# Kernel tuning notes

Measured on AMD Instinct MI355X. Metric: run time of the kernel, lower is better.

## Reference

```python
import jax, jax.numpy as jnp
import numpy as np
from jax import lax

EPS = 1e-5
TEM = 10.0  # self.tem at init; tem_proportion buffer is 0 so it stays 10.0


def _conv1d(x, w, padding, dilation=1, groups=1):
    # x: [B, C, S], w: [O, I//groups, K]
    return lax.conv_general_dilated(
        x, w, window_strides=(1,), padding=[(padding, padding)],
        rhs_dilation=(dilation,), dimension_numbers=('NCH', 'OIH', 'NCH'),
        feature_group_count=groups)


def _bn(y, gamma, beta):
    # training-mode BatchNorm1d: stats over (batch, length) per channel
    m = y.mean(axis=(0, 2), keepdims=True)
    v = y.var(axis=(0, 2), keepdims=True)
    return (y - m) * lax.rsqrt(v + EPS) * gamma[None, :, None] + beta[None, :, None]


def _nor_conv(x, w, g, b, k):
    return _bn(_conv1d(jax.nn.relu(x), w, padding=k // 2), g, b)


def _dil_conv(x, wd, wp, g, b, k):
    C = x.shape[1]
    y = _conv1d(jax.nn.relu(x), wd, padding=k - 1, dilation=2, groups=C)
    y = _conv1d(y, wp, padding=0)
    return _bn(y, g, b)


def _avg_pool3(x):
    s = lax.reduce_window(x, 0.0, lax.add, (1, 1, 3), (1, 1, 1),
                          [(0, 0), (0, 0), (1, 1)])
    return s / 3.0  # count_include_pad=True


def _max_pool3(x):
    return lax.reduce_window(x, -jnp.inf, lax.max, (1, 1, 3), (1, 1, 1),
                             [(0, 0), (0, 0), (1, 1)])


def _forward(x, u, arch_parameters,
             w_nor3, g_nor3, b_nor3, w_nor5, g_nor5, b_nor5,
             w_nor7, g_nor7, b_nor7,
             wd_dil3, wp_dil3, g_dil3, b_dil3,
             wd_dil5, wp_dil5, g_dil5, b_dil5,
             wd_dil7, wp_dil7, g_dil7, b_dil7):
    # ---- Gumbel straight-through gate (get_gumbel_prob) ----
    uc = jnp.clip(u, 1e-9, 1.0 - 1e-9)
    gumbels = -jnp.log(-jnp.log(uc))  # -log(Exp(1) sample)
    logits = (jax.nn.log_softmax(arch_parameters, axis=1) + gumbels) / TEM
    probs = jax.nn.softmax(logits, axis=1)          # [1, 10]
    index = jnp.argmax(probs, axis=-1)              # [1]
    one_h = jax.nn.one_hot(index, probs.shape[-1], dtype=probs.dtype)
    hardwts = one_h - lax.stop_gradient(probs) + probs  # straight-through

    # ---- forward_gdas: single edge (max_nodes=2) ----
    xc = jnp.transpose(x, (0, 2, 1))  # [B, H, S]: hidden=channels, seq=length
    branches = [
        lambda t: jnp.zeros_like(t),                         # none
        _avg_pool3,                                          # avg_pool_3
        _max_pool3,                                          # max_pool_3
        lambda t: _nor_conv(t, w_nor3, g_nor3, b_nor3, 3),   # nor_conv_3
        lambda t: _nor_conv(t, w_nor5, g_nor5, b_nor5, 5),   # nor_conv_5
        lambda t: _nor_conv(t, w_nor7, g_nor7, b_nor7, 7),   # nor_conv_7
        lambda t: _dil_conv(t, wd_dil3, wp_dil3, g_dil3, b_dil3, 3),
        lambda t: _dil_conv(t, wd_dil5, wp_dil5, g_dil5, b_dil5, 5),
        lambda t: _dil_conv(t, wd_dil7, wp_dil7, g_dil7, b_dil7, 7),
        lambda t: t,                                         # skip_connect
    ]
    idx = index[0]
    w = hardwts[0]                                  # [10]
    sel = lax.switch(idx, branches, xc)             # only argmax op is run
    w_sel = jnp.take(w, idx)
    # GDAS: w[argmax]*op(x) + sum of remaining scalar weights (broadcast add)
    out = w_sel * sel + (jnp.sum(w) - w_sel)
    out = jnp.transpose(out, (0, 2, 1))             # back to [B, S, H]
    return out + x                                  # residual


def setup_inputs() -> dict:
    key = jax.random.key(0)
    ks = jax.random.split(key, 16)
    B, S, H = 8, 512, 768
    d = {
        'x': jax.random.normal(ks[0], (B, S, H), jnp.float32),
        'u': jax.random.uniform(ks[1], (1, 10), jnp.float32),
        'arch_parameters': 0.001 * jax.random.normal(ks[2], (1, 10), jnp.float32),
    }
    i = 3
    for k in (3, 5, 7):
        d[f'w_nor{k}'] = 0.02 * jax.random.normal(ks[i], (H, H, k), jnp.float32); i += 1
        d[f'g_nor{k}'] = jnp.ones((H,), jnp.float32)
        d[f'b_nor{k}'] = jnp.zeros((H,), jnp.float32)
    for k in (3, 5, 7):
        d[f'wd_dil{k}'] = 0.1 * jax.random.normal(ks[i], (H, 1, k), jnp.float32); i += 1
        d[f'wp_dil{k}'] = 0.02 * jax.random.normal(ks[i], (H, H, 1), jnp.float32); i += 1
        d[f'g_dil{k}'] = jnp.ones((H,), jnp.float32)
        d[f'b_dil{k}'] = jnp.zeros((H,), jnp.float32)
    return d


def reference(x, u, arch_parameters,
              w_nor3, g_nor3, b_nor3, w_nor5, g_nor5, b_nor5,
              w_nor7, g_nor7, b_nor7,
              wd_dil3, wp_dil3, g_dil3, b_dil3,
              wd_dil5, wp_dil5, g_dil5, b_dil5,
              wd_dil7, wp_dil7, g_dil7, b_dil7):
    return _forward(x, u, arch_parameters,
                    w_nor3, g_nor3, b_nor3, w_nor5, g_nor5, b_nor5,
                    w_nor7, g_nor7, b_nor7,
                    wd_dil3, wp_dil3, g_dil3, b_dil3,
                    wd_dil5, wp_dil5, g_dil5, b_dil5,
                    wd_dil7, wp_dil7, g_dil7, b_dil7)
```

## Files before the change

kernel.cpp:

```cpp
#include <hip/hip_runtime.h>
#include <math.h>

#define BB 8
#define SS 512
#define HH 768
#define NTOT (BB*SS*HH)
#define EPSBN 1e-5f
#define SPAD 4
#define SROWS (SS + 2*SPAD)

typedef __attribute__((ext_vector_type(8))) short short8v;
typedef __attribute__((ext_vector_type(4))) float float4v;

struct Params {
  const float *x, *u, *ap;
  const float *w_nor3, *g_nor3, *b_nor3;
  const float *w_nor5, *g_nor5, *b_nor5;
  const float *w_nor7, *g_nor7, *b_nor7;
  const float *wd3, *wp3, *gd3, *bd3;
  const float *wd5, *wp5, *gd5, *bd5;
  const float *wd7, *wp7, *gd7, *bd7;
  float *out;
  float *hdr;
  float *y;
  short *xb;
  short *wb;
  float *psum;
  float *psq;
};

__device__ __forceinline__ short f2bf(float f) {
  union { float f; unsigned u; } v; v.f = f;
  unsigned r = v.u + 0x7FFF + ((v.u >> 16) & 1);
  return (short)(r >> 16);
}

__global__ void gate_kernel(Params p) {
  int t = threadIdx.x;
  for (int i = t; i < HH; i += 64) { p.psum[i] = 0.f; p.psq[i] = 0.f; }
  if (t != 0) return;
  float ap[10], lg[10], pr[10];
  float mx = -INFINITY;
  for (int i = 0; i < 10; i++) { ap[i] = p.ap[i]; mx = fmaxf(mx, ap[i]); }
  float se = 0.f;
  for (int i = 0; i < 10; i++) se += expf(ap[i] - mx);
  float lse = mx + logf(se);
  float lmax = -INFINITY;
  for (int i = 0; i < 10; i++) {
    float uc = fminf(fmaxf(p.u[i], 1e-9f), 1.f - 1e-9f);
    float gb = -logf(-logf(uc));
    lg[i] = ((ap[i] - lse) + gb) * 0.1f;
    lmax = fmaxf(lmax, lg[i]);
  }
  float ps = 0.f;
  for (int i = 0; i < 10; i++) { pr[i] = expf(lg[i] - lmax); ps += pr[i]; }
  int idx = 0; float best = -INFINITY;
  for (int i = 0; i < 10; i++) {
    pr[i] /= ps;
    if (pr[i] > best) { best = pr[i]; idx = i; }
  }
  float w_sel = (1.0f - pr[idx]) + pr[idx];
  p.hdr[0] = w_sel;
  p.hdr[1] = 0.0f;
  ((int*)p.hdr)[2] = idx;
}

#define XBLK 1560
#define WBLK 288

template<int K>
__device__ __forceinline__ void wprep(const float* __restrict__ W, short* __restrict__ wb,
                                      int o, int i0) {
  const float* src = W + ((size_t)o * HH + i0) * K;
  float f[8 * K];
#pragma unroll
  for (int j = 0; j < 2 * K; j++) ((float4*)f)[j] = ((const float4*)src)[j];
#pragma unroll
  for (int dk = 0; dk < K; dk++) {
    short8v o8;
#pragma unroll
    for (int j = 0; j < 8; j++) o8[j] = f2bf(f[j * K + dk]);
    *(short8v*)(wb + ((size_t)dk * HH + o) * HH + i0) = o8;
  }
}

__global__ __launch_bounds__(256) void prep_kernel(Params p) {
  int idx = ((const int*)p.hdr)[2];
  if (idx < 3 || idx > 8) return;
  int t = threadIdx.x;
  if (blockIdx.x < XBLK) {
    int u = blockIdx.x * 256 + t;
    int c0 = (u % 96) * 8;
    int row = (u / 96) % SROWS;
    int b = u / (96 * SROWS);
    int s = row - SPAD;
    short8v o8 = (short8v){0,0,0,0,0,0,0,0};
    if (s >= 0 && s < SS) {
      float v[8];
      if (idx <= 5) {
        const float* xp = p.x + ((size_t)(b * SS + s) * HH + c0);
        float4 f0 = ((const float4*)xp)[0];
        float4 f1 = ((const float4*)xp)[1];
        v[0] = fmaxf(f0.x, 0.f); v[1] = fmaxf(f0.y, 0.f);
        v[2] = fmaxf(f0.z, 0.f); v[3] = fmaxf(f0.w, 0.f);
        v[4] = fmaxf(f1.x, 0.f); v[5] = fmaxf(f1.y, 0.f);
        v[6] = fmaxf(f1.z, 0.f); v[7] = fmaxf(f1.w, 0.f);
      } else {
        int k = 3 + 2 * (idx - 6);
        const float* wd = (idx == 6) ? p.wd3 : (idx == 7) ? p.wd5 : p.wd7;
#pragma unroll
        for (int j = 0; j < 8; j++) v[j] = 0.f;
        for (int dk = 0; dk < k; dk++) {
          int ss = s + 2 * dk - (k - 1);
          if (ss < 0 || ss >= SS) continue;
          const float* xp = p.x + ((size_t)(b * SS + ss) * HH + c0);
          float4 f0 = ((const float4*)xp)[0];
          float4 f1 = ((const float4*)xp)[1];
          float ff[8] = {f0.x, f0.y, f0.z, f0.w, f1.x, f1.y, f1.z, f1.w};
#pragma unroll
          for (int j = 0; j < 8; j++)
            v[j] += fmaxf(ff[j], 0.f) * wd[(c0 + j) * k + dk];
        }
      }
#pragma unroll
      for (int j = 0; j < 8; j++) o8[j] = f2bf(v[j]);
    }
    *(short8v*)(p.xb + (size_t)(b * SROWS + row) * HH + c0) = o8;
  } else {
    int u = (blockIdx.x - XBLK) * 256 + t;
    int i0 = (u % 96) * 8;
    int o = u / 96;
    if (idx == 3)      wprep<3>(p.w_nor3, p.wb, o, i0);
    else if (idx == 4) wprep<5>(p.w_nor5, p.wb, o, i0);
    else if (idx == 5) wprep<7>(p.w_nor7, p.wb, o, i0);
    else wprep<1>((idx == 6) ? p.wp3 : (idx == 7) ? p.wp5 : p.wp7, p.wb, o, i0);
  }
}

#define BM 128
#define BN 64
#define BK 64
#define AROWS 136

typedef const __attribute__((address_space(1))) unsigned int* gas_t;
typedef __attribute__((address_space(3))) unsigned int* las_t;
__device__ __forceinline__ void gload16(const void* g, void* l) {
  __builtin_amdgcn_global_load_lds((gas_t)g, (las_t)l, 16, 0, 0);
}

__global__ __launch_bounds__(256, 3) void conv_gemm_kernel(Params p) {
  int idx = ((const int*)p.hdr)[2];
  if (idx < 3 || idx > 8) return;
  bool nor = (idx <= 5);
  int taps = nor ? (3 + 2 * (idx - 3)) : 1;
  int halo = nor ? (taps >> 1) : 0;

  __shared__ __attribute__((aligned(16))) short As[AROWS * BK];
  __shared__ __attribute__((aligned(16))) short Bs[4 * BN * BK];

  int mt = blockIdx.x;
  int b = mt >> 2;
  int s0 = (mt & 3) * BM;
  int o0 = blockIdx.y * BN;

  int t = threadIdx.x;
  int lane = t & 63;
  int w = t >> 6;
  int l16 = lane & 15, quad = lane >> 4;
  int wm0 = (w >> 1) * 64;
  int wn0 = (w & 1) * 32;
  int lr = lane >> 3;
  int sw8 = ((lane & 7) ^ lr) * 8;

  const short* Ag[4];
  int abrow = b * SROWS + s0 + 8 * w + lr;
#pragma unroll
  for (int j = 0; j < 4; j++)
    Ag[j] = p.xb + (size_t)(abrow + 32 * j) * HH + sw8;
  const short* Agp = p.xb + (size_t)(b * SROWS + s0 + 128 + lr) * HH + sw8;
  const short* Bg = p.wb + (size_t)(o0 + 8 * w + lr) * HH + sw8;

  short* Asl[4];
#pragma unroll
  for (int j = 0; j < 4; j++) Asl[j] = &As[(32 * j + 8 * w) * BK];
  short* Aslp = &As[128 * BK];

  float4v acc[4][2];
#pragma unroll
  for (int mi = 0; mi < 4; mi++)
#pragma unroll
    for (int ni = 0; ni < 2; ni++) acc[mi][ni] = (float4v){0.f, 0.f, 0.f, 0.f};

  const char* Ac = (const char*)As;
  const char* Bc = (const char*)Bs;
  int bb[2][2];
#pragma unroll
  for (int ni = 0; ni < 2; ni++)
#pragma unroll
    for (int h = 0; h < 2; h++)
      bb[ni][h] = (wn0 + ni * 16 + l16) * (2 * BK) + (((h * 4 + quad) ^ (l16 & 7)) << 4);

  int np0 = taps < 4 ? taps : 4;
  int np1 = taps - np0;

  auto mm = [&](int dk, int pl) {
    int doff = dk - halo + 4;
    int rowA = wm0 + l16 + doff;
    int xr = (l16 + doff) & 7;
    int a0 = rowA * 128 + ((quad ^ xr) << 4);
    int a1 = rowA * 128 + (((4 + quad) ^ xr) << 4);
    short8v af0[4], af1[4], bf0[2], bf1[2];
#pragma unroll
    for (int mi = 0; mi < 4; mi++) {
      af0[mi] = *(const short8v*)(Ac + a0 + mi * 2048);
      af1[mi] = *(const short8v*)(Ac + a1 + mi * 2048);
    }
    int pb = pl * 8192;
#pragma unroll
    for (int ni = 0; ni < 2; ni++) {
      bf0[ni] = *(const short8v*)(Bc + pb + bb[ni][0]);
      bf1[ni] = *(const short8v*)(Bc + pb + bb[ni][1]);
    }
#pragma unroll
    for (int mi = 0; mi < 4; mi++)
#pragma unroll
      for (int ni = 0; ni < 2; ni++)
        acc[mi][ni] = __builtin_amdgcn_mfma_f32_16x16x32_bf16(af0[mi], bf0[ni], acc[mi][ni], 0, 0, 0);
#pragma unroll
    for (int mi = 0; mi < 4; mi++)
#pragma unroll
      for (int ni = 0; ni < 2; ni++)
        acc[mi][ni] = __builtin_amdgcn_mfma_f32_16x16x32_bf16(af1[mi], bf1[ni], acc[mi][ni], 0, 0, 0);
  };

  for (int k0 = 0; k0 < HH; k0 += BK) {
#pragma unroll
    for (int j = 0; j < 4; j++) gload16(Ag[j] + k0, Asl[j]);
    if (w == 0) gload16(Agp + k0, Aslp);
    for (int pl = 0; pl < np0; pl++) {
      const short* src = Bg + (size_t)pl * HH * HH + k0;
      gload16(src, &Bs[pl * 4096 + w * 512]);
      gload16(src + (size_t)32 * HH, &Bs[pl * 4096 + 2048 + w * 512]);
    }
    __syncthreads();
    for (int dk = 0; dk < np0; dk++) mm(dk, dk);
    __syncthreads();
    if (np1 > 0) {
      for (int pl = 0; pl < np1; pl++) {
        const short* src = Bg + (size_t)(4 + pl) * HH * HH + k0;
        gload16(src, &Bs[pl * 4096 + w * 512]);
        gload16(src + (size_t)32 * HH, &Bs[pl * 4096 + 2048 + w * 512]);
      }
      __syncthreads();
      for (int dk = 0; dk < np1; dk++) mm(4 + dk, dk);
      __syncthreads();
    }
  }

#pragma unroll
  for (int mi = 0; mi < 4; mi++)
#pragma unroll
    for (int ni = 0; ni < 2; ni++) {
      int col = o0 + wn0 + ni * 16 + l16;
#pragma unroll
      for (int r = 0; r < 4; r++) {
        int row = s0 + wm0 + mi * 16 + quad * 4 + r;
        p.y[((size_t)(b * SS + row)) * HH + col] = acc[mi][ni][r];
      }
    }

#pragma unroll
  for (int ni = 0; ni < 2; ni++) {
    float s = 0.f, q = 0.f;
#pragma unroll
    for (int mi = 0; mi < 4; mi++)
#pragma unroll
      for (int r = 0; r < 4; r++) { float v = acc[mi][ni][r]; s += v; q += v * v; }
    s += __shfl_xor(s, 16); s += __shfl_xor(s, 32);
    q += __shfl_xor(q, 16); q += __shfl_xor(q, 32);
    if (lane < 16) {
      int col = o0 + wn0 + ni * 16 + l16;
      atomicAdd(&p.psum[col], s);
      atomicAdd(&p.psq[col], q);
    }
  }
}

__global__ __launch_bounds__(256) void epilogue_kernel(Params p) {
  int idx = ((const int*)p.hdr)[2];
  float w_sel = p.hdr[0], w_rest = p.hdr[1];
  int t4 = blockIdx.x * 256 + threadIdx.x;
  int base = t4 * 4;
  float4 xv = *(const float4*)(p.x + base);
  float4 sel;
  if (idx >= 3 && idx <= 8) {
    const float* g = (idx == 3) ? p.g_nor3 : (idx == 4) ? p.g_nor5 : (idx == 5) ? p.g_nor7
                   : (idx == 6) ? p.gd3 : (idx == 7) ? p.gd5 : p.gd7;
    const float* be = (idx == 3) ? p.b_nor3 : (idx == 4) ? p.b_nor5 : (idx == 5) ? p.b_nor7
                    : (idx == 6) ? p.bd3 : (idx == 7) ? p.bd5 : p.bd7;
    int c = base % HH;
    float4 yv = *(const float4*)(p.y + base);
    float4 ps = *(const float4*)(p.psum + c);
    float4 pq = *(const float4*)(p.psq + c);
    float4 gv = *(const float4*)(g + c);
    float4 bv = *(const float4*)(be + c);
    const float inv = 1.f / 4096.f;
    float m0 = ps.x * inv, m1 = ps.y * inv, m2 = ps.z * inv, m3 = ps.w * inv;
    float i0 = rsqrtf(pq.x * inv - m0 * m0 + EPSBN);
    float i1 = rsqrtf(pq.y * inv - m1 * m1 + EPSBN);
    float i2 = rsqrtf(pq.z * inv - m2 * m2 + EPSBN);
    float i3 = rsqrtf(pq.w * inv - m3 * m3 + EPSBN);
    sel.x = (yv.x - m0) * i0 * gv.x + bv.x;
    sel.y = (yv.y - m1) * i1 * gv.y + bv.y;
    sel.z = (yv.z - m2) * i2 * gv.z + bv.z;
    sel.w = (yv.w - m3) * i3 * gv.w + bv.w;
  } else if (idx == 0) {
    sel = (float4){0.f, 0.f, 0.f, 0.f};
  } else if (idx == 9) {
    sel = xv;
  } else {
    int s = (base / HH) % SS;
    float4 xm, xp;
    if (idx == 1) {
      xm = (s > 0)      ? *(const float4*)(p.x + base - HH) : (float4){0.f, 0.f, 0.f, 0.f};
      xp = (s < SS - 1) ? *(const float4*)(p.x + base + HH) : (float4){0.f, 0.f, 0.f, 0.f};
      const float th = 1.f / 3.f;
      sel.x = (xm.x + xv.x + xp.x) * th;
      sel.y = (xm.y + xv.y + xp.y) * th;
      sel.z = (xm.z + xv.z + xp.z) * th;
      sel.w = (xm.w + xv.w + xp.w) * th;
    } else {
      xm = (s > 0)      ? *(const float4*)(p.x + base - HH) : (float4){-INFINITY, -INFINITY, -INFINITY, -INFINITY};
      xp = (s < SS - 1) ? *(const float4*)(p.x + base + HH) : (float4){-INFINITY, -INFINITY, -INFINITY, -INFINITY};
      sel.x = fmaxf(fmaxf(xm.x, xv.x), xp.x);
      sel.y = fmaxf(fmaxf(xm.y, xv.y), xp.y);
      sel.z = fmaxf(fmaxf(xm.z, xv.z), xp.z);
      sel.w = fmaxf(fmaxf(xm.w, xv.w), xp.w);
    }
  }
  float4 ov;
  ov.x = w_sel * sel.x + w_rest + xv.x;
  ov.y = w_sel * sel.y + w_rest + xv.y;
  ov.z = w_sel * sel.z + w_rest + xv.z;
  ov.w = w_sel * sel.w + w_rest + xv.w;
  *(float4*)(p.out + base) = ov;
}

extern "C" void kernel_launch(void* const* d_in, const int* in_sizes, int n_in,
                              void* d_out, int out_size, void* d_ws, size_t ws_size,
                              hipStream_t stream) {
  Params p;
  p.x = (const float*)d_in[0];
  p.u = (const float*)d_in[1];
  p.ap = (const float*)d_in[2];
  p.w_nor3 = (const float*)d_in[3];  p.g_nor3 = (const float*)d_in[4];  p.b_nor3 = (const float*)d_in[5];
  p.w_nor5 = (const float*)d_in[6];  p.g_nor5 = (const float*)d_in[7];  p.b_nor5 = (const float*)d_in[8];
  p.w_nor7 = (const float*)d_in[9];  p.g_nor7 = (const float*)d_in[10]; p.b_nor7 = (const float*)d_in[11];
  p.wd3 = (const float*)d_in[12]; p.wp3 = (const float*)d_in[13]; p.gd3 = (const float*)d_in[14]; p.bd3 = (const float*)d_in[15];
  p.wd5 = (const float*)d_in[16]; p.wp5 = (const float*)d_in[17]; p.gd5 = (const float*)d_in[18]; p.bd5 = (const float*)d_in[19];
  p.wd7 = (const float*)d_in[20]; p.wp7 = (const float*)d_in[21]; p.gd7 = (const float*)d_in[22]; p.bd7 = (const float*)d_in[23];
  p.out = (float*)d_out;

  char* ws = (char*)d_ws;
  size_t off = 0;
  p.hdr = (float*)(ws + off); off += 256;
  p.y   = (float*)(ws + off); off += (size_t)NTOT * 4;
  p.xb  = (short*)(ws + off); off += (size_t)BB * SROWS * HH * 2;
  p.wb  = (short*)(ws + off); off += (size_t)7 * HH * HH * 2;
  p.psum = (float*)(ws + off); off += HH * 4;
  p.psq  = (float*)(ws + off); off += HH * 4;

  hipLaunchKernelGGL(gate_kernel, dim3(1), dim3(64), 0, stream, p);
  hipLaunchKernelGGL(prep_kernel, dim3(XBLK + WBLK), dim3(256), 0, stream, p);
  hipLaunchKernelGGL(conv_gemm_kernel, dim3(SS * BB / BM, HH / BN), dim3(256), 0, stream, p);
  hipLaunchKernelGGL(epilogue_kernel, dim3(NTOT / 4 / 256), dim3(256), 0, stream, p);
}
```

Before: 137.1 us.

## Fold gate computation into prep kernel and use grid-stride loops

Removes the separate single-thread gate kernel launch by recomputing the Gumbel gate in every prep block, with block 0 writing the header and zeroing the BN stat accumulators. Prep and epilogue kernels switch to fixed-size grids with grid-stride loops instead of one thread per item. This saves a launch and the serialized tiny kernel, at the cost of redundant per-block gate math (transcendentals on thread 0 before a barrier). It also relies on the conv kernel launching after prep has finished zeroing psum.

```diff
diff --git a/kernel.cpp b/kernel.cpp
--- a/kernel.cpp
+++ b/kernel.cpp
@@ -35,19 +35,18 @@
   return (short)(r >> 16);
 }
 
-__global__ void gate_kernel(Params p) {
-  int t = threadIdx.x;
-  for (int i = t; i < HH; i += 64) { p.psum[i] = 0.f; p.psq[i] = 0.f; }
-  if (t != 0) return;
+__device__ __forceinline__ void gate_compute(const float* __restrict__ apg,
+                                             const float* __restrict__ ug,
+                                             int& idx_out, float& wsel_out) {
   float ap[10], lg[10], pr[10];
   float mx = -INFINITY;
-  for (int i = 0; i < 10; i++) { ap[i] = p.ap[i]; mx = fmaxf(mx, ap[i]); }
+  for (int i = 0; i < 10; i++) { ap[i] = apg[i]; mx = fmaxf(mx, ap[i]); }
   float se = 0.f;
   for (int i = 0; i < 10; i++) se += expf(ap[i] - mx);
   float lse = mx + logf(se);
   float lmax = -INFINITY;
   for (int i = 0; i < 10; i++) {
-    float uc = fminf(fmaxf(p.u[i], 1e-9f), 1.f - 1e-9f);
+    float uc = fminf(fmaxf(ug[i], 1e-9f), 1.f - 1e-9f);
     float gb = -logf(-logf(uc));
     lg[i] = ((ap[i] - lse) + gb) * 0.1f;
     lmax = fmaxf(lmax, lg[i]);
@@ -59,14 +58,13 @@
     pr[i] /= ps;
     if (pr[i] > best) { best = pr[i]; idx = i; }
   }
-  float w_sel = (1.0f - pr[idx]) + pr[idx];
-  p.hdr[0] = w_sel;
-  p.hdr[1] = 0.0f;
-  ((int*)p.hdr)[2] = idx;
-}
-
-#define XBLK 1560
-#define WBLK 288
+  idx_out = idx;
+  wsel_out = (1.0f - pr[idx]) + pr[idx];
+}
+
+#define NITEMS_A (BB * SROWS * 96)
+#define NITEMS   (NITEMS_A + HH * 96)
+#define PREP_BLOCKS 512
 
 template<int K>
 __device__ __forceinline__ void wprep(const float* __restrict__ W, short* __restrict__ wb,
@@ -85,55 +83,73 @@
 }
 
 __global__ __launch_bounds__(256) void prep_kernel(Params p) {
-  int idx = ((const int*)p.hdr)[2];
+  __shared__ int sh_idx;
+  int t = threadIdx.x;
+  if (t == 0) {
+    int idx; float wsel;
+    gate_compute(p.ap, p.u, idx, wsel);
+    sh_idx = idx;
+    if (blockIdx.x == 0) {
+      p.hdr[0] = wsel;
+      p.hdr[1] = 0.0f;
+      ((int*)p.hdr)[2] = idx;
+    }
+  }
+  __syncthreads();
+  int idx = sh_idx;
   if (idx < 3 || idx > 8) return;
-  int t = threadIdx.x;
-  if (blockIdx.x < XBLK) {
-    int u = blockIdx.x * 256 + t;
-    int c0 = (u % 96) * 8;
-    int row = (u / 96) % SROWS;
-    int b = u / (96 * SROWS);
-    int s = row - SPAD;
-    short8v o8 = (short8v){0,0,0,0,0,0,0,0};
-    if (s >= 0 && s < SS) {
-      float v[8];
-      if (idx <= 5) {
-        const float* xp = p.x + ((size_t)(b * SS + s) * HH + c0);
-        float4 f0 = ((const float4*)xp)[0];
-        float4 f1 = ((const float4*)xp)[1];
-        v[0] = fmaxf(f0.x, 0.f); v[1] = fmaxf(f0.y, 0.f);
-        v[2] = fmaxf(f0.z, 0.f); v[3] = fmaxf(f0.w, 0.f);
-        v[4] = fmaxf(f1.x, 0.f); v[5] = fmaxf(f1.y, 0.f);
-        v[6] = fmaxf(f1.z, 0.f); v[7] = fmaxf(f1.w, 0.f);
-      } else {
-        int k = 3 + 2 * (idx - 6);
-        const float* wd = (idx == 6) ? p.wd3 : (idx == 7) ? p.wd5 : p.wd7;
-#pragma unroll
-        for (int j = 0; j < 8; j++) v[j] = 0.f;
-        for (int dk = 0; dk < k; dk++) {
-          int ss = s + 2 * dk - (k - 1);
-          if (ss < 0 || ss >= SS) continue;
-          const float* xp = p.x + ((size_t)(b * SS + ss) * HH + c0);
+
+  if (blockIdx.x == 0) {
+    for (int i = t; i < HH; i += 256) { p.psum[i] = 0.f; p.psq[i] = 0.f; }
+  }
+
+  for (int u = blockIdx.x * 256 + t; u < NITEMS; u += PREP_BLOCKS * 256) {
+    if (u < NITEMS_A) {
+      int c0 = (u % 96) * 8;
+      int row = (u / 96) % SROWS;
+      int b = u / (96 * SROWS);
+      int s = row - SPAD;
+      short8v o8 = (short8v){0,0,0,0,0,0,0,0};
+      if (s >= 0 && s < SS) {
+        float v[8];
+        if (idx <= 5) {
+          const float* xp = p.x + ((size_t)(b * SS + s) * HH + c0);
           float4 f0 = ((const float4*)xp)[0];
           float4 f1 = ((const float4*)xp)[1];
-          float ff[8] = {f0.x, f0.y, f0.z, f0.w, f1.x, f1.y, f1.z, f1.w};
-#pragma unroll
-          for (int j = 0; j < 8; j++)
-            v[j] += fmaxf(ff[j], 0.f) * wd[(c0 + j) * k + dk];
+          v[0] = fmaxf(f0.x, 0.f); v[1] = fmaxf(f0.y, 0.f);
+          v[2] = fmaxf(f0.z, 0.f); v[3] = fmaxf(f0.w, 0.f);
+          v[4] = fmaxf(f1.x, 0.f); v[5] = fmaxf(f1.y, 0.f);
+          v[6] = fmaxf(f1.z, 0.f); v[7] = fmaxf(f1.w, 0.f);
+        } else {
+          int k = 3 + 2 * (idx - 6);
+          const float* wd = (idx == 6) ? p.wd3 : (idx == 7) ? p.wd5 : p.wd7;
+#pragma unroll
+          for (int j = 0; j < 8; j++) v[j] = 0.f;
+          for (int dk = 0; dk < k; dk++) {
+            int ss = s + 2 * dk - (k - 1);
+            if (ss < 0 || ss >= SS) continue;
+            const float* xp = p.x + ((size_t)(b * SS + ss) * HH + c0);
+            float4 f0 = ((const float4*)xp)[0];
+            float4 f1 = ((const float4*)xp)[1];
+            float ff[8] = {f0.x, f0.y, f0.z, f0.w, f1.x, f1.y, f1.z, f1.w};
+#pragma unroll
+            for (int j = 0; j < 8; j++)
+              v[j] += fmaxf(ff[j], 0.f) * wd[(c0 + j) * k + dk];
+          }
         }
+#pragma unroll
+        for (int j = 0; j < 8; j++) o8[j] = f2bf(v[j]);
       }
-#pragma unroll
-      for (int j = 0; j < 8; j++) o8[j] = f2bf(v[j]);
-    }
-    *(short8v*)(p.xb + (size_t)(b * SROWS + row) * HH + c0) = o8;
-  } else {
-    int u = (blockIdx.x - XBLK) * 256 + t;
-    int i0 = (u % 96) * 8;
-    int o = u / 96;
-    if (idx == 3)      wprep<3>(p.w_nor3, p.wb, o, i0);
-    else if (idx == 4) wprep<5>(p.w_nor5, p.wb, o, i0);
-    else if (idx == 5) wprep<7>(p.w_nor7, p.wb, o, i0);
-    else wprep<1>((idx == 6) ? p.wp3 : (idx == 7) ? p.wp5 : p.wp7, p.wb, o, i0);
+      *(short8v*)(p.xb + (size_t)(b * SROWS + row) * HH + c0) = o8;
+    } else {
+      int u2 = u - NITEMS_A;
+      int i0 = (u2 % 96) * 8;
+      int o = u2 / 96;
+      if (idx == 3)      wprep<3>(p.w_nor3, p.wb, o, i0);
+      else if (idx == 4) wprep<5>(p.w_nor5, p.wb, o, i0);
+      else if (idx == 5) wprep<7>(p.w_nor7, p.wb, o, i0);
+      else wprep<1>((idx == 6) ? p.wp3 : (idx == 7) ? p.wp5 : p.wp7, p.wb, o, i0);
+    }
   }
 }
 
@@ -286,64 +302,65 @@
   }
 }
 
+#define EPI_BLOCKS 1536
 __global__ __launch_bounds__(256) void epilogue_kernel(Params p) {
   int idx = ((const int*)p.hdr)[2];
   float w_sel = p.hdr[0], w_rest = p.hdr[1];
-  int t4 = blockIdx.x * 256 + threadIdx.x;
-  int base = t4 * 4;
-  float4 xv = *(const float4*)(p.x + base);
-  float4 sel;
-  if (idx >= 3 && idx <= 8) {
-    const float* g = (idx == 3) ? p.g_nor3 : (idx == 4) ? p.g_nor5 : (idx == 5) ? p.g_nor7
-                   : (idx == 6) ? p.gd3 : (idx == 7) ? p.gd5 : p.gd7;
-    const float* be = (idx == 3) ? p.b_nor3 : (idx == 4) ? p.b_nor5 : (idx == 5) ? p.b_nor7
-                    : (idx == 6) ? p.bd3 : (idx == 7) ? p.bd5 : p.bd7;
-    int c = base % HH;
-    float4 yv = *(const float4*)(p.y + base);
-    float4 ps = *(const float4*)(p.psum + c);
-    float4 pq = *(const float4*)(p.psq + c);
-    float4 gv = *(const float4*)(g + c);
-    float4 bv = *(const float4*)(be + c);
-    const float inv = 1.f / 4096.f;
-    float m0 = ps.x * inv, m1 = ps.y * inv, m2 = ps.z * inv, m3 = ps.w * inv;
-    float i0 = rsqrtf(pq.x * inv - m0 * m0 + EPSBN);
-    float i1 = rsqrtf(pq.y * inv - m1 * m1 + EPSBN);
-    float i2 = rsqrtf(pq.z * inv - m2 * m2 + EPSBN);
-    float i3 = rsqrtf(pq.w * inv - m3 * m3 + EPSBN);
-    sel.x = (yv.x - m0) * i0 * gv.x + bv.x;
-    sel.y = (yv.y - m1) * i1 * gv.y + bv.y;
-    sel.z = (yv.z - m2) * i2 * gv.z + bv.z;
-    sel.w = (yv.w - m3) * i3 * gv.w + bv.w;
-  } else if (idx == 0) {
-    sel = (float4){0.f, 0.f, 0.f, 0.f};
-  } else if (idx == 9) {
-    sel = xv;
-  } else {
-    int s = (base / HH) % SS;
-    float4 xm, xp;
-    if (idx == 1) {
-      xm = (s > 0)      ? *(const float4*)(p.x + base - HH) : (float4){0.f, 0.f, 0.f, 0.f};
-      xp = (s < SS - 1) ? *(const float4*)(p.x + base + HH) : (float4){0.f, 0.f, 0.f, 0.f};
-      const float th = 1.f / 3.f;
-      sel.x = (xm.x + xv.x + xp.x) * th;
-      sel.y = (xm.y + xv.y + xp.y) * th;
-      sel.z = (xm.z + xv.z + xp.z) * th;
-      sel.w = (xm.w + xv.w + xp.w) * th;
+  for (int t4 = blockIdx.x * 256 + threadIdx.x; t4 < NTOT / 4; t4 += EPI_BLOCKS * 256) {
+    int base = t4 * 4;
+    float4 xv = *(const float4*)(p.x + base);
+    float4 sel;
+    if (idx >= 3 && idx <= 8) {
+      const float* g = (idx == 3) ? p.g_nor3 : (idx == 4) ? p.g_nor5 : (idx == 5) ? p.g_nor7
+                     : (idx == 6) ? p.gd3 : (idx == 7) ? p.gd5 : p.gd7;
+      const float* be = (idx == 3) ? p.b_nor3 : (idx == 4) ? p.b_nor5 : (idx == 5) ? p.b_nor7
+                      : (idx == 6) ? p.bd3 : (idx == 7) ? p.bd5 : p.bd7;
+      int c = base % HH;
+      float4 yv = *(const float4*)(p.y + base);
+      float4 ps = *(const float4*)(p.psum + c);
+      float4 pq = *(const float4*)(p.psq + c);
+      float4 gv = *(const float4*)(g + c);
+      float4 bv = *(const float4*)(be + c);
+      const float inv = 1.f / 4096.f;
+      float m0 = ps.x * inv, m1 = ps.y * inv, m2 = ps.z * inv, m3 = ps.w * inv;
+      float i0 = rsqrtf(pq.x * inv - m0 * m0 + EPSBN);
+      float i1 = rsqrtf(pq.y * inv - m1 * m1 + EPSBN);
+      float i2 = rsqrtf(pq.z * inv - m2 * m2 + EPSBN);
+      float i3 = rsqrtf(pq.w * inv - m3 * m3 + EPSBN);
+      sel.x = (yv.x - m0) * i0 * gv.x + bv.x;
+      sel.y = (yv.y - m1) * i1 * gv.y + bv.y;
+      sel.z = (yv.z - m2) * i2 * gv.z + bv.z;
+      sel.w = (yv.w - m3) * i3 * gv.w + bv.w;
+    } else if (idx == 0) {
+      sel = (float4){0.f, 0.f, 0.f, 0.f};
+    } else if (idx == 9) {
+      sel = xv;
     } else {
-      xm = (s > 0)      ? *(const float4*)(p.x + base - HH) : (float4){-INFINITY, -INFINITY, -INFINITY, -INFINITY};
-      xp = (s < SS - 1) ? *(const float4*)(p.x + base + HH) : (float4){-INFINITY, -INFINITY, -INFINITY, -INFINITY};
-      sel.x = fmaxf(fmaxf(xm.x, xv.x), xp.x);
-      sel.y = fmaxf(fmaxf(xm.y, xv.y), xp.y);
-      sel.z = fmaxf(fmaxf(xm.z, xv.z), xp.z);
-      sel.w = fmaxf(fmaxf(xm.w, xv.w), xp.w);
-    }
-  }
-  float4 ov;
-  ov.x = w_sel * sel.x + w_rest + xv.x;
-  ov.y = w_sel * sel.y + w_rest + xv.y;
-  ov.z = w_sel * sel.z + w_rest + xv.z;
-  ov.w = w_sel * sel.w + w_rest + xv.w;
-  *(float4*)(p.out + base) = ov;
+      int s = (base / HH) % SS;
+      float4 xm, xp;
+      if (idx == 1) {
+        xm = (s > 0)      ? *(const float4*)(p.x + base - HH) : (float4){0.f, 0.f, 0.f, 0.f};
+        xp = (s < SS - 1) ? *(const float4*)(p.x + base + HH) : (float4){0.f, 0.f, 0.f, 0.f};
+        sel.x = (xm.x + xv.x + xp.x) / 3.f;
+        sel.y = (xm.y + xv.y + xp.y) / 3.f;
+        sel.z = (xm.z + xv.z + xp.z) / 3.f;
+        sel.w = (xm.w + xv.w + xp.w) / 3.f;
+      } else {
+        xm = (s > 0)      ? *(const float4*)(p.x + base - HH) : (float4){-INFINITY, -INFINITY, -INFINITY, -INFINITY};
+        xp = (s < SS - 1) ? *(const float4*)(p.x + base + HH) : (float4){-INFINITY, -INFINITY, -INFINITY, -INFINITY};
+        sel.x = fmaxf(fmaxf(xm.x, xv.x), xp.x);
+        sel.y = fmaxf(fmaxf(xm.y, xv.y), xp.y);
+        sel.z = fmaxf(fmaxf(xm.z, xv.z), xp.z);
+        sel.w = fmaxf(fmaxf(xm.w, xv.w), xp.w);
+      }
+    }
+    float4 ov;
+    ov.x = w_sel * sel.x + w_rest + xv.x;
+    ov.y = w_sel * sel.y + w_rest + xv.y;
+    ov.z = w_sel * sel.z + w_rest + xv.z;
+    ov.w = w_sel * sel.w + w_rest + xv.w;
+    *(float4*)(p.out + base) = ov;
+  }
 }
 
 extern "C" void kernel_launch(void* const* d_in, const int* in_sizes, int n_in,
@@ -370,8 +387,7 @@
   p.psum = (float*)(ws + off); off += HH * 4;
   p.psq  = (float*)(ws + off); off += HH * 4;
 
-  hipLaunchKernelGGL(gate_kernel, dim3(1), dim3(64), 0, stream, p);
-  hipLaunchKernelGGL(prep_kernel, dim3(XBLK + WBLK), dim3(256), 0, stream, p);
+  hipLaunchKernelGGL(prep_kernel, dim3(PREP_BLOCKS), dim3(256), 0, stream, p);
   hipLaunchKernelGGL(conv_gemm_kernel, dim3(SS * BB / BM, HH / BN), dim3(256), 0, stream, p);
-  hipLaunchKernelGGL(epilogue_kernel, dim3(NTOT / 4 / 256), dim3(256), 0, stream, p);
-}
+  hipLaunchKernelGGL(epilogue_kernel, dim3(EPI_BLOCKS), dim3(256), 0, stream, p);
+}
```

Measured after the change: 134.7 us. Within noise of the previous version (-1.7%).
